# Kernel optimization log

Measured on AMD Instinct MI355X. Metric: run time of the kernel, lower is better.

## Reference

```python
import jax, jax.numpy as jnp
import numpy as np

N_ROWS = 8192
EMBED_DIM = 256


def setup_inputs() -> dict:
    key = jax.random.key(0)
    k1, k2, k3, k4, k5 = jax.random.split(key, 5)
    M = jax.random.normal(k1, (N_ROWS, EMBED_DIM), dtype=jnp.float32)
    N = jax.random.normal(k2, (N_ROWS, EMBED_DIM), dtype=jnp.float32)
    # gate_w: nn.Linear(embed_dim, 1) -> weight [1, d], bias [1]; gate_b extra scalar param [1]
    Wg = jax.random.normal(k3, (1, EMBED_DIM), dtype=jnp.float32) * 0.06
    bg = jax.random.normal(k4, (1,), dtype=jnp.float32) * 0.1
    gate_b = jax.random.normal(k5, (1,), dtype=jnp.float32) * 0.1
    return {"M": M, "N": N, "Wg": Wg, "bg": bg, "gate_b": gate_b, "iseval": 0}


def reference(M, N, Wg, bg, gate_b, iseval):
    # mt: [n, n] cross-similarity scores
    mt = jnp.matmul(N, M.T)
    if not iseval:
        # training branch: zero out the diagonal (mt - diag(diag(mt)))
        n = mt.shape[0]
        idx = jnp.arange(n)
        mt = mt.at[idx, idx].set(0.0)
    else:
        # eval branch: zero out the first row
        mt = mt.at[0].set(0.0)
    attn_weight = jax.nn.softmax(mt, axis=-1)          # [n, n]
    out_attn = jnp.matmul(attn_weight, M)              # [n, d]
    gate = jax.nn.sigmoid(jnp.matmul(out_attn, Wg.T) + bg + gate_b)  # [n, 1]
    boosted = out_attn * gate + N * (1.0 - gate)       # [n, d]
    return boosted[:, None, None, :]                   # [n, 1, 1, d]
```

## Files before the change

### kernel.cpp

```cpp
#include <hip/hip_runtime.h>


constexpr int EMBED = 256;
constexpr int BQ = 64;
constexpr int BJ = 32;
constexpr int NT = 256;

constexpr int SS_OFF = 0;
constexpr int SS_BUF = 18432;
constexpr int PH_OFF = 36864;
constexpr int PH_BUF = 5120;
constexpr int AS_OFF = 47104;
constexpr int AS_BUF = 256;
constexpr int LDS_SZ = 47616;

typedef _Float16 half8 __attribute__((ext_vector_type(8)));
typedef float f32x4 __attribute__((ext_vector_type(4)));
typedef short short8v __attribute__((ext_vector_type(8)));

static __device__ __forceinline__ f32x4 mfma16(half8 a, half8 b, f32x4 c) {
    return __builtin_amdgcn_mfma_f32_16x16x32_f16(a, b, c, 0, 0, 0);
}
static __device__ __forceinline__ short f2h(float x) {
    return (short)__builtin_bit_cast(unsigned short, (_Float16)x);
}
static __device__ __forceinline__ void barrier_lds() {
    asm volatile("s_waitcnt lgkmcnt(0)" ::: "memory");
    __builtin_amdgcn_s_barrier();
    __builtin_amdgcn_sched_barrier(0);
}

__global__ void prep(const float* __restrict__ M,
                     short* __restrict__ MhG, short* __restrict__ MtG) {
    __shared__ float L[16 * 260];
    const int r0 = blockIdx.x * 16;
    const int t = threadIdx.x;
    const int pj = t >> 4, pc = (t & 15) * 16;
    {
        const float* src = M + (size_t)(r0 + pj) * EMBED + pc;
        float4 v[4];
        #pragma unroll
        for (int i = 0; i < 4; ++i) v[i] = ((const float4*)src)[i];
        short* hd = MhG + (size_t)(r0 + pj) * EMBED + pc;
        #pragma unroll
        for (int i = 0; i < 2; ++i) {
            float4 a = v[2 * i], b = v[2 * i + 1];
            short8v h;
            h[0]=f2h(a.x); h[1]=f2h(a.y); h[2]=f2h(a.z); h[3]=f2h(a.w);
            h[4]=f2h(b.x); h[5]=f2h(b.y); h[6]=f2h(b.z); h[7]=f2h(b.w);
            *(short8v*)(hd + 8 * i) = h;
        }
        #pragma unroll
        for (int i = 0; i < 4; ++i)
            *(float4*)(L + pj * 260 + pc + 4 * i) = v[i];
    }
    __syncthreads();
    {
        const int d = t;
        const int tile = r0 >> 5, jh = (r0 >> 4) & 1;
        short* dst = MtG + (size_t)tile * (BJ * EMBED) + d * BJ + jh * 16;
        #pragma unroll
        for (int g2 = 0; g2 < 2; ++g2) {
            short8v w;
            #pragma unroll
            for (int e = 0; e < 8; ++e) w[e] = f2h(L[(g2 * 8 + e) * 260 + d]);
            *(short8v*)(dst + g2 * 8) = w;
        }
    }
}

__launch_bounds__(NT, 2)
__global__ void attn(const short* __restrict__ MhG, const short* __restrict__ MtG,
                     const float* __restrict__ Ng, const int* __restrict__ iseval_p,
                     float* __restrict__ O0out, short* __restrict__ Ofp,
                     float* __restrict__ MLm, float* __restrict__ MLl, int n)
{
    __shared__ __align__(16) char smem[LDS_SZ];

    const int t = threadIdx.x, lane = t & 63, wave = t >> 6;
    const int quad = lane >> 4, mn = lane & 15;
    const int bid = blockIdx.x;
    const int s  = (bid & 7) >> 1;
    const int qb = ((bid >> 3) << 1) | (bid & 1);
    const int q0 = qb * BQ;
    const int jbase = s * (n >> 2);
    const int jb32 = jbase / BJ;
    const int ntiles = (n >> 2) / BJ;
    const int iseval = *iseval_p;
    const int jt = wave & 1, kh = wave >> 1;
    const int dq = wave;
    const int sq = t >> 2, sh = t & 3;

    const float L2E = 1.4426950408889634f;
    half8 Qf[4][4];
    #pragma unroll
    for (int qi = 0; qi < 4; ++qi) {
        const float* np = Ng + (size_t)(q0 + qi * 16 + mn) * EMBED;
        #pragma unroll
        for (int kk = 0; kk < 4; ++kk) {
            const float* p = np + (kh * 4 + kk) * 32 + quad * 8;
            float4 a = *(const float4*)p, b = *(const float4*)(p + 4);
            half8 h;
            h[0]=(_Float16)(a.x*L2E); h[1]=(_Float16)(a.y*L2E);
            h[2]=(_Float16)(a.z*L2E); h[3]=(_Float16)(a.w*L2E);
            h[4]=(_Float16)(b.x*L2E); h[5]=(_Float16)(b.y*L2E);
            h[6]=(_Float16)(b.z*L2E); h[7]=(_Float16)(b.w*L2E);
            Qf[qi][kk] = h;
        }
    }

    f32x4 O[4][4];
    #pragma unroll
    for (int qi = 0; qi < 4; ++qi)
        #pragma unroll
        for (int dt = 0; dt < 4; ++dt) O[qi][dt] = (f32x4){0.f, 0.f, 0.f, 0.f};

    float m_reg = -1e30f, l_reg = 0.f;

    const short* mhb0 = MhG + (size_t)(jbase + jt * 16 + mn) * EMBED + kh * 128 + quad * 8;
    half8 Bc[4], Bn[4], Mtf[4];
    #pragma unroll
    for (int kk = 0; kk < 4; ++kk) Bc[kk] = *(const half8*)(mhb0 + kk * 32);

    __syncthreads();

    for (int tt = 0; tt <= ntiles; ++tt) {
        const int bw = tt & 1;
        const int br = bw ^ 1;

        if (tt > 0) {
            const short* mtb = MtG + (size_t)(jb32 + (tt - 1)) * (BJ * EMBED);
            #pragma unroll
            for (int dt = 0; dt < 4; ++dt)
                Mtf[dt] = *(const half8*)(mtb + (dq * 64 + dt * 16 + mn) * BJ + quad * 8);
        }

        if (tt < ntiles) {
            f32x4 a0 = (f32x4){0,0,0,0}, a1 = (f32x4){0,0,0,0};
            f32x4 a2 = (f32x4){0,0,0,0}, a3 = (f32x4){0,0,0,0};
            #pragma unroll
            for (int kk = 0; kk < 4; ++kk) {
                half8 bf = Bc[kk];
                a0 = mfma16(Qf[0][kk], bf, a0);
                a1 = mfma16(Qf[1][kk], bf, a1);
                a2 = mfma16(Qf[2][kk], bf, a2);
                a3 = mfma16(Qf[3][kk], bf, a3);
            }
            float* ssp = (float*)(smem + SS_OFF + bw * SS_BUF) + kh * 2304;
            #pragma unroll
            for (int r = 0; r < 4; ++r) {
                ssp[(0  + quad * 4 + r) * 36 + jt * 16 + mn] = a0[r];
                ssp[(16 + quad * 4 + r) * 36 + jt * 16 + mn] = a1[r];
                ssp[(32 + quad * 4 + r) * 36 + jt * 16 + mn] = a2[r];
                ssp[(48 + quad * 4 + r) * 36 + jt * 16 + mn] = a3[r];
            }
        }

        if (tt + 1 < ntiles) {
            const short* nb = mhb0 + (size_t)(tt + 1) * (BJ * EMBED);
            #pragma unroll
            for (int kk = 0; kk < 4; ++kk) Bn[kk] = *(const half8*)(nb + kk * 32);
        }

        if (tt > 0) {
            const int j0g = jbase + (tt - 1) * BJ;
            const float* p0 = (const float*)(smem + SS_OFF + br * SS_BUF) + sq * 36 + 8 * sh;
            float4 sa = *(const float4*)p0;
            float4 sb = *(const float4*)(p0 + 4);
            float4 sc = *(const float4*)(p0 + 2304);
            float4 sd = *(const float4*)(p0 + 2308);
            float sv[8] = {sa.x + sc.x, sa.y + sc.y, sa.z + sc.z, sa.w + sc.w,
                           sb.x + sd.x, sb.y + sd.y, sb.z + sd.z, sb.w + sd.w};
            const int qg = q0 + sq;
            if (iseval) {
                if (qg == 0) {
                    #pragma unroll
                    for (int i = 0; i < 8; ++i) sv[i] = 0.f;
                }
            } else {
                int dj = qg - j0g - 8 * sh;
                #pragma unroll
                for (int i = 0; i < 8; ++i) if (dj == i) sv[i] = 0.f;
            }
            float mx = sv[0];
            #pragma unroll
            for (int i = 1; i < 8; ++i) mx = fmaxf(mx, sv[i]);
            mx = fmaxf(mx, __shfl_xor(mx, 1));
            mx = fmaxf(mx, __shfl_xor(mx, 2));
            float m_new = fmaxf(m_reg, mx);
            float alpha = exp2f(m_reg - m_new);
            float p[8], ps = 0.f;
            #pragma unroll
            for (int i = 0; i < 8; ++i) { p[i] = exp2f(sv[i] - m_new); ps += p[i]; }
            ps += __shfl_xor(ps, 1);
            ps += __shfl_xor(ps, 2);
            m_reg = m_new;
            l_reg = l_reg * alpha + ps;
            if (sh == 0)
                ((float*)(smem + AS_OFF + br * AS_BUF))[sq] = alpha;
            half8 ph;
            #pragma unroll
            for (int i = 0; i < 8; ++i) ph[i] = (_Float16)p[i];
            *(half8*)(smem + PH_OFF + br * PH_BUF + sq * 80 + sh * 16) = ph;
        }

        barrier_lds();

        if (tt > 0) {
            #pragma unroll
            for (int qi = 0; qi < 4; ++qi) {
                half8 pf = *(const half8*)(smem + PH_OFF + br * PH_BUF + (qi * 16 + mn) * 80 + quad * 16);
                f32x4 al = *(const f32x4*)((const float*)(smem + AS_OFF + br * AS_BUF) + qi * 16 + quad * 4);
                #pragma unroll
                for (int dt = 0; dt < 4; ++dt) {
                    f32x4 o = O[qi][dt];
                    o[0] *= al[0]; o[1] *= al[1]; o[2] *= al[2]; o[3] *= al[3];
                    O[qi][dt] = mfma16(pf, Mtf[dt], o);
                }
            }
        }

        #pragma unroll
        for (int kk = 0; kk < 4; ++kk) Bc[kk] = Bn[kk];
    }

    if (s == 0) {
        #pragma unroll
        for (int qi = 0; qi < 4; ++qi)
            #pragma unroll
            for (int dt = 0; dt < 4; ++dt) {
                int col = dq * 64 + dt * 16 + mn;
                #pragma unroll
                for (int r = 0; r < 4; ++r)
                    O0out[(size_t)(q0 + qi * 16 + quad * 4 + r) * EMBED + col] = O[qi][dt][r];
            }
    } else {
        short* dst = Ofp + (size_t)(s - 1) * n * EMBED;
        #pragma unroll
        for (int qi = 0; qi < 4; ++qi)
            #pragma unroll
            for (int dt = 0; dt < 4; ++dt) {
                int col = dq * 64 + dt * 16 + mn;
                #pragma unroll
                for (int r = 0; r < 4; ++r)
                    dst[(size_t)(q0 + qi * 16 + quad * 4 + r) * EMBED + col] = f2h(O[qi][dt][r]);
            }
    }
    if (sh == 0) {
        MLm[s * n + q0 + sq] = m_reg;
        MLl[s * n + q0 + sq] = l_reg;
    }
}

__global__ void combine4(const float* __restrict__ O0, const short* __restrict__ Ofp,
                         const float* __restrict__ MLm, const float* __restrict__ MLl,
                         const float* __restrict__ Ng, const float* __restrict__ Wg,
                         const float* __restrict__ bg, const float* __restrict__ gb,
                         float* __restrict__ out, int n)
{
    const int t = threadIdx.x;
    const int row = blockIdx.x * 16 + (t >> 4);
    const int c = t & 15;
    float ms[4], ls[4];
    #pragma unroll
    for (int k = 0; k < 4; ++k) { ms[k] = MLm[k * n + row]; ls[k] = MLl[k * n + row]; }
    float m = fmaxf(fmaxf(ms[0], ms[1]), fmaxf(ms[2], ms[3]));
    float w[4], lsum = 0.f;
    #pragma unroll
    for (int k = 0; k < 4; ++k) { w[k] = exp2f(ms[k] - m); lsum += w[k] * ls[k]; }
    float linv = 1.f / lsum;

    float acc[16];
    {
        const float4* o0 = (const float4*)(O0 + (size_t)row * EMBED + c * 16);
        #pragma unroll
        for (int i = 0; i < 4; ++i) {
            float4 v = o0[i];
            acc[4*i+0] = w[0] * v.x; acc[4*i+1] = w[0] * v.y;
            acc[4*i+2] = w[0] * v.z; acc[4*i+3] = w[0] * v.w;
        }
    }
    #pragma unroll
    for (int k = 1; k < 4; ++k) {
        const short* op = Ofp + (size_t)(k - 1) * n * EMBED + (size_t)row * EMBED + c * 16;
        half8 a = *(const half8*)op, b = *(const half8*)(op + 8);
        #pragma unroll
        for (int i = 0; i < 8; ++i) {
            acc[i]     += w[k] * (float)a[i];
            acc[8 + i] += w[k] * (float)b[i];
        }
    }
    float dot = 0.f;
    #pragma unroll
    for (int i = 0; i < 16; ++i) { acc[i] *= linv; dot += acc[i] * Wg[c * 16 + i]; }
    dot += __shfl_xor(dot, 1);
    dot += __shfl_xor(dot, 2);
    dot += __shfl_xor(dot, 4);
    dot += __shfl_xor(dot, 8);
    float g = 1.f / (1.f + __expf(-(dot + bg[0] + gb[0])));
    const float4* n4 = (const float4*)(Ng + (size_t)row * EMBED + c * 16);
    float4* o4 = (float4*)(out + (size_t)row * EMBED + c * 16);
    #pragma unroll
    for (int i = 0; i < 4; ++i) {
        float4 nn = n4[i];
        float4 res;
        res.x = acc[4*i+0] * g + nn.x * (1.f - g);
        res.y = acc[4*i+1] * g + nn.y * (1.f - g);
        res.z = acc[4*i+2] * g + nn.z * (1.f - g);
        res.w = acc[4*i+3] * g + nn.w * (1.f - g);
        o4[i] = res;
    }
}

extern "C" void kernel_launch(void* const* d_in, const int* in_sizes, int n_in,
                              void* d_out, int out_size, void* d_ws, size_t ws_size,
                              hipStream_t stream) {
    const float* M      = (const float*)d_in[0];
    const float* N      = (const float*)d_in[1];
    const float* Wgp    = (const float*)d_in[2];
    const float* bgp    = (const float*)d_in[3];
    const float* gbp    = (const float*)d_in[4];
    const int*   iseval = (const int*)d_in[5];
    float* out = (float*)d_out;

    int n = in_sizes[0] / EMBED;
    short* MhG = (short*)d_ws;
    short* MtG = MhG + (size_t)n * EMBED;
    short* Ofp = MtG + (size_t)n * EMBED;
    float* MLm = (float*)(Ofp + (size_t)3 * n * EMBED);
    float* MLl = MLm + 4 * n;

    hipLaunchKernelGGL(prep, dim3(n / 16), dim3(NT), 0, stream, M, MhG, MtG);
    hipLaunchKernelGGL(attn, dim3((n / BQ) * 4), dim3(NT), 0, stream,
                       MhG, MtG, N, iseval, out, Ofp, MLm, MLl, n);
    hipLaunchKernelGGL(combine4, dim3(n / 16), dim3(NT), 0, stream,
                       out, Ofp, MLm, MLl, N, Wgp, bgp, gbp, out, n);
}
```

Measured before the change: 186.5 us.

## Fuse split-KV combine and gating into attention via last-block atomic counter

Removes the separate combine4 kernel and instead has each attention block increment a per-query-block atomic counter after writing its partial results. The fourth block to finish for a query block merges the four split partials, applies the sigmoid gate and writes the output. This saves one kernel launch and lets the combine work overlap with other attention blocks. In exchange it adds a memset, threadfences and a serial combine tail inside the attention kernel.

```diff
diff --git a/kernel.cpp b/kernel.cpp
--- a/kernel.cpp
+++ b/kernel.cpp
@@ -73,9 +73,12 @@
 __global__ void attn(const short* __restrict__ MhG, const short* __restrict__ MtG,
                      const float* __restrict__ Ng, const int* __restrict__ iseval_p,
                      float* __restrict__ O0out, short* __restrict__ Ofp,
-                     float* __restrict__ MLm, float* __restrict__ MLl, int n)
+                     float* __restrict__ MLm, float* __restrict__ MLl,
+                     const float* __restrict__ Wg, const float* __restrict__ bg,
+                     const float* __restrict__ gb, int* __restrict__ cnt, int n)
 {
     __shared__ __align__(16) char smem[LDS_SZ];
+    __shared__ int lastFlag;
 
     const int t = threadIdx.x, lane = t & 63, wave = t >> 6;
     const int quad = lane >> 4, mn = lane & 15;
@@ -250,65 +253,70 @@
         MLm[s * n + q0 + sq] = m_reg;
         MLl[s * n + q0 + sq] = l_reg;
     }
-}
-
-__global__ void combine4(const float* __restrict__ O0, const short* __restrict__ Ofp,
-                         const float* __restrict__ MLm, const float* __restrict__ MLl,
-                         const float* __restrict__ Ng, const float* __restrict__ Wg,
-                         const float* __restrict__ bg, const float* __restrict__ gb,
-                         float* __restrict__ out, int n)
-{
-    const int t = threadIdx.x;
-    const int row = blockIdx.x * 16 + (t >> 4);
-    const int c = t & 15;
-    float ms[4], ls[4];
-    #pragma unroll
-    for (int k = 0; k < 4; ++k) { ms[k] = MLm[k * n + row]; ls[k] = MLl[k * n + row]; }
-    float m = fmaxf(fmaxf(ms[0], ms[1]), fmaxf(ms[2], ms[3]));
-    float w[4], lsum = 0.f;
-    #pragma unroll
-    for (int k = 0; k < 4; ++k) { w[k] = exp2f(ms[k] - m); lsum += w[k] * ls[k]; }
-    float linv = 1.f / lsum;
-
-    float acc[16];
-    {
-        const float4* o0 = (const float4*)(O0 + (size_t)row * EMBED + c * 16);
-        #pragma unroll
-        for (int i = 0; i < 4; ++i) {
-            float4 v = o0[i];
-            acc[4*i+0] = w[0] * v.x; acc[4*i+1] = w[0] * v.y;
-            acc[4*i+2] = w[0] * v.z; acc[4*i+3] = w[0] * v.w;
-        }
-    }
-    #pragma unroll
-    for (int k = 1; k < 4; ++k) {
-        const short* op = Ofp + (size_t)(k - 1) * n * EMBED + (size_t)row * EMBED + c * 16;
-        half8 a = *(const half8*)op, b = *(const half8*)(op + 8);
-        #pragma unroll
-        for (int i = 0; i < 8; ++i) {
-            acc[i]     += w[k] * (float)a[i];
-            acc[8 + i] += w[k] * (float)b[i];
-        }
-    }
-    float dot = 0.f;
-    #pragma unroll
-    for (int i = 0; i < 16; ++i) { acc[i] *= linv; dot += acc[i] * Wg[c * 16 + i]; }
-    dot += __shfl_xor(dot, 1);
-    dot += __shfl_xor(dot, 2);
-    dot += __shfl_xor(dot, 4);
-    dot += __shfl_xor(dot, 8);
-    float g = 1.f / (1.f + __expf(-(dot + bg[0] + gb[0])));
-    const float4* n4 = (const float4*)(Ng + (size_t)row * EMBED + c * 16);
-    float4* o4 = (float4*)(out + (size_t)row * EMBED + c * 16);
-    #pragma unroll
-    for (int i = 0; i < 4; ++i) {
-        float4 nn = n4[i];
-        float4 res;
-        res.x = acc[4*i+0] * g + nn.x * (1.f - g);
-        res.y = acc[4*i+1] * g + nn.y * (1.f - g);
-        res.z = acc[4*i+2] * g + nn.z * (1.f - g);
-        res.w = acc[4*i+3] * g + nn.w * (1.f - g);
-        o4[i] = res;
+
+    __threadfence();
+    __syncthreads();
+    if (t == 0) {
+        int old = atomicAdd(&cnt[qb], 1);
+        lastFlag = (old == 3);
+    }
+    __syncthreads();
+    if (lastFlag) {
+        __threadfence();
+        #pragma unroll 1
+        for (int pass = 0; pass < 4; ++pass) {
+            const int row = q0 + pass * 16 + (t >> 4);
+            const int c = t & 15;
+            float ms[4], ls[4];
+            #pragma unroll
+            for (int k = 0; k < 4; ++k) { ms[k] = MLm[k * n + row]; ls[k] = MLl[k * n + row]; }
+            float m = fmaxf(fmaxf(ms[0], ms[1]), fmaxf(ms[2], ms[3]));
+            float w[4], lsum = 0.f;
+            #pragma unroll
+            for (int k = 0; k < 4; ++k) { w[k] = exp2f(ms[k] - m); lsum += w[k] * ls[k]; }
+            float linv = 1.f / lsum;
+
+            float acc[16];
+            {
+                const float4* o0 = (const float4*)(O0out + (size_t)row * EMBED + c * 16);
+                #pragma unroll
+                for (int i = 0; i < 4; ++i) {
+                    float4 v = o0[i];
+                    acc[4*i+0] = w[0] * v.x; acc[4*i+1] = w[0] * v.y;
+                    acc[4*i+2] = w[0] * v.z; acc[4*i+3] = w[0] * v.w;
+                }
+            }
+            #pragma unroll
+            for (int k = 1; k < 4; ++k) {
+                const short* op = Ofp + (size_t)(k - 1) * n * EMBED + (size_t)row * EMBED + c * 16;
+                half8 a = *(const half8*)op, b = *(const half8*)(op + 8);
+                #pragma unroll
+                for (int i = 0; i < 8; ++i) {
+                    acc[i]     += w[k] * (float)a[i];
+                    acc[8 + i] += w[k] * (float)b[i];
+                }
+            }
+            float dot = 0.f;
+            #pragma unroll
+            for (int i = 0; i < 16; ++i) { acc[i] *= linv; dot += acc[i] * Wg[c * 16 + i]; }
+            dot += __shfl_xor(dot, 1);
+            dot += __shfl_xor(dot, 2);
+            dot += __shfl_xor(dot, 4);
+            dot += __shfl_xor(dot, 8);
+            float g = 1.f / (1.f + __expf(-(dot + bg[0] + gb[0])));
+            const float4* n4 = (const float4*)(Ng + (size_t)row * EMBED + c * 16);
+            float4* o4 = (float4*)(O0out + (size_t)row * EMBED + c * 16);
+            #pragma unroll
+            for (int i = 0; i < 4; ++i) {
+                float4 nn = n4[i];
+                float4 res;
+                res.x = acc[4*i+0] * g + nn.x * (1.f - g);
+                res.y = acc[4*i+1] * g + nn.y * (1.f - g);
+                res.z = acc[4*i+2] * g + nn.z * (1.f - g);
+                res.w = acc[4*i+3] * g + nn.w * (1.f - g);
+                o4[i] = res;
+            }
+        }
     }
 }
 
@@ -329,10 +337,11 @@
     short* Ofp = MtG + (size_t)n * EMBED;
     float* MLm = (float*)(Ofp + (size_t)3 * n * EMBED);
     float* MLl = MLm + 4 * n;
-
+    int*   cnt = (int*)(MLl + 4 * n);
+
+    hipMemsetAsync(cnt, 0, (n / BQ) * sizeof(int), stream);
     hipLaunchKernelGGL(prep, dim3(n / 16), dim3(NT), 0, stream, M, MhG, MtG);
     hipLaunchKernelGGL(attn, dim3((n / BQ) * 4), dim3(NT), 0, stream,
-                       MhG, MtG, N, iseval, out, Ofp, MLm, MLl, n);
-    hipLaunchKernelGGL(combine4, dim3(n / 16), dim3(NT), 0, stream,
-                       out, Ofp, MLm, MLl, N, Wgp, bgp, gbp, out, n);
-}
+                       MhG, MtG, N, iseval, out, Ofp, MLm, MLl,
+                       Wgp, bgp, gbp, cnt, n);
+}
```

Result: slower. 309.1 us (+65.7%).
